# Kernel optimization log

Measured on AMD Instinct MI355X. Metric: run time of the kernel, lower is better.

## Reference

```python
import jax, jax.numpy as jnp
import numpy as np

N = 50000   # nodes
E = 800000  # edges
D = 64      # num_filters == hidden_channels
NG = 5      # num_gaussians (edge_attr width, unused by forward math)
NEG_SLOPE = 0.2


def setup_inputs() -> dict:
    key = jax.random.key(0)
    ks = jax.random.split(key, 16)
    s = 1.0 / np.sqrt(D)
    return {
        "x": jax.random.normal(ks[0], (N, D), dtype=jnp.float32),
        "edge_index": jax.random.randint(ks[1], (2, E), 0, N, dtype=jnp.int64),
        "edge_weight": jax.random.uniform(ks[2], (E,), dtype=jnp.float32),
        "edge_attr": jax.random.normal(ks[3], (E, NG), dtype=jnp.float32),
        "W0": jax.random.normal(ks[4], (D, D), dtype=jnp.float32) * s,
        "b0": jnp.zeros((D,), dtype=jnp.float32),
        "W1": jax.random.normal(ks[5], (D, D), dtype=jnp.float32) * s,
        "as1": jax.random.normal(ks[6], (D,), dtype=jnp.float32) * s,
        "ad1": jax.random.normal(ks[7], (D,), dtype=jnp.float32) * s,
        "b1": jnp.zeros((D,), dtype=jnp.float32),
        "W2": jax.random.normal(ks[8], (D, D), dtype=jnp.float32) * s,
        "as2": jax.random.normal(ks[9], (D,), dtype=jnp.float32) * s,
        "ad2": jax.random.normal(ks[10], (D,), dtype=jnp.float32) * s,
        "b2": jnp.zeros((D,), dtype=jnp.float32),
    }


def gat_layer(h, src, dst, W, a_src, a_dst, b):
    # PyG GATConv, heads=1, add_self_loops=False
    hx = h @ W  # [N, D]
    # per-node attention logits, gathered per edge (edge j->i: src=j, dst=i)
    alpha = (hx * a_src).sum(-1)[src] + (hx * a_dst).sum(-1)[dst]  # [E]
    alpha = jax.nn.leaky_relu(alpha, NEG_SLOPE)
    # segment softmax grouped by destination node
    m = jax.ops.segment_max(alpha, dst, num_segments=N)
    e = jnp.exp(alpha - m[dst])
    s = jax.ops.segment_sum(e, dst, num_segments=N)
    p = e / s[dst]  # [E]
    # scatter-add weighted source features
    out = jax.ops.segment_sum(hx[src] * p[:, None], dst, num_segments=N)
    return out + b


def reference(x, edge_index, edge_weight, edge_attr,
              W0, b0, W1, as1, ad1, b1, W2, as2, ad2, b2):
    # edge_weight / edge_attr are accepted but unused, as in the torch module
    src, dst = edge_index[0], edge_index[1]
    out = jax.nn.relu(x @ W0 + b0)
    out = out + jax.nn.relu(gat_layer(out, src, dst, W1, as1, ad1, b1))
    out = out + jax.nn.relu(gat_layer(out, src, dst, W2, as2, ad2, b2))
    return out
```

## Files before the change

### kernel.cpp

```cpp
#include <hip/hip_runtime.h>
#include <hip/hip_bf16.h>

#define DD 64
#define NEG_SLOPE 0.2f
#define HS 68
#define CAP 64
#define BSH 8
#define BN  256
#define NBMAX 256
#define NBLK 256
#define STAGE_CAP 6144

__device__ __forceinline__ unsigned short f2bf(float f)
{
    unsigned u = __float_as_uint(f);
    u += 0x7FFFu + ((u >> 16) & 1u);
    return (unsigned short)(u >> 16);
}
__device__ __forceinline__ float bf2f(unsigned short b)
{
    return __uint_as_float(((unsigned)b) << 16);
}

__global__ __launch_bounds__(256) void mm_fused(
    const float* __restrict__ x,
    const float* __restrict__ W0, const float* __restrict__ b0,
    const float* __restrict__ W1,
    const float* __restrict__ a_src, const float* __restrict__ a_dst,
    float* __restrict__ h, ushort4* __restrict__ hxb4,
    float* __restrict__ sarr, float* __restrict__ darr, int n)
{
    __shared__ float Wsh[DD * DD];
    __shared__ float Hsh[DD * HS];
    int tid = threadIdx.x;
    for (int i = tid * 4; i < DD * DD; i += 1024)
        *(float4*)&Wsh[i] = *(const float4*)&W0[i];

    int fg = tid & 15, ng = tid >> 4;
    int tile0 = blockIdx.x * 64;
    for (int p = 0; p < 4; ++p) {
        int nl = p * 16 + ng, gn = tile0 + nl;
        if (gn < n)
            *(float4*)&Hsh[nl * HS + 4 * fg] = *(const float4*)&x[gn * DD + 4 * fg];
    }
    __syncthreads();

    float4 acc[4];
#pragma unroll
    for (int j = 0; j < 4; ++j) acc[j] = float4{0.f, 0.f, 0.f, 0.f};
#pragma unroll 8
    for (int k = 0; k < DD; ++k) {
        float4 w4 = *(float4*)&Wsh[k * DD + 4 * fg];
#pragma unroll
        for (int j = 0; j < 4; ++j) {
            float hv = Hsh[(4 * ng + j) * HS + k];
            acc[j].x += hv * w4.x; acc[j].y += hv * w4.y;
            acc[j].z += hv * w4.z; acc[j].w += hv * w4.w;
        }
    }

    float4 b4 = *(const float4*)&b0[4 * fg];
    float4 o[4];
#pragma unroll
    for (int j = 0; j < 4; ++j) {
        o[j].x = fmaxf(acc[j].x + b4.x, 0.f);
        o[j].y = fmaxf(acc[j].y + b4.y, 0.f);
        o[j].z = fmaxf(acc[j].z + b4.z, 0.f);
        o[j].w = fmaxf(acc[j].w + b4.w, 0.f);
        int gn = tile0 + 4 * ng + j;
        if (gn < n) *(float4*)&h[gn * DD + 4 * fg] = o[j];
    }
    __syncthreads();

#pragma unroll
    for (int j = 0; j < 4; ++j)
        *(float4*)&Hsh[(4 * ng + j) * HS + 4 * fg] = o[j];
    for (int i = tid * 4; i < DD * DD; i += 1024)
        *(float4*)&Wsh[i] = *(const float4*)&W1[i];
    __syncthreads();

#pragma unroll
    for (int j = 0; j < 4; ++j) acc[j] = float4{0.f, 0.f, 0.f, 0.f};
#pragma unroll 8
    for (int k = 0; k < DD; ++k) {
        float4 w4 = *(float4*)&Wsh[k * DD + 4 * fg];
#pragma unroll
        for (int j = 0; j < 4; ++j) {
            float hv = Hsh[(4 * ng + j) * HS + k];
            acc[j].x += hv * w4.x; acc[j].y += hv * w4.y;
            acc[j].z += hv * w4.z; acc[j].w += hv * w4.w;
        }
    }

    float4 as4 = *(const float4*)&a_src[4 * fg];
    float4 ad4 = *(const float4*)&a_dst[4 * fg];
#pragma unroll
    for (int j = 0; j < 4; ++j) {
        int gn = tile0 + 4 * ng + j;
        if (gn < n) {
            ushort4 hb;
            hb.x = f2bf(acc[j].x); hb.y = f2bf(acc[j].y);
            hb.z = f2bf(acc[j].z); hb.w = f2bf(acc[j].w);
            hxb4[gn * 16 + fg] = hb;
        }
        float ps = acc[j].x * as4.x + acc[j].y * as4.y + acc[j].z * as4.z + acc[j].w * as4.w;
        float pd = acc[j].x * ad4.x + acc[j].y * ad4.y + acc[j].z * ad4.z + acc[j].w * ad4.w;
#pragma unroll
        for (int off = 8; off; off >>= 1) {
            ps += __shfl_xor(ps, off);
            pd += __shfl_xor(pd, off);
        }
        if (fg == 0 && gn < n) { sarr[gn] = ps; darr[gn] = pd; }
    }
}

__global__ __launch_bounds__(256) void mm_gat(
    const float* __restrict__ h, const float* __restrict__ W,
    const float* __restrict__ a_src, const float* __restrict__ a_dst,
    ushort4* __restrict__ hxb4, float* __restrict__ sarr, float* __restrict__ darr,
    int n)
{
    __shared__ float Wsh[DD * DD];
    __shared__ float Hsh[DD * HS];
    int tid = threadIdx.x;
    for (int i = tid * 4; i < DD * DD; i += 1024)
        *(float4*)&Wsh[i] = *(const float4*)&W[i];

    int fg = tid & 15, ng = tid >> 4;
    int tile0 = blockIdx.x * 64;
    for (int p = 0; p < 4; ++p) {
        int nl = p * 16 + ng, gn = tile0 + nl;
        if (gn < n)
            *(float4*)&Hsh[nl * HS + 4 * fg] = *(const float4*)&h[gn * DD + 4 * fg];
    }
    __syncthreads();

    float4 acc[4];
#pragma unroll
    for (int j = 0; j < 4; ++j) acc[j] = float4{0.f, 0.f, 0.f, 0.f};
#pragma unroll 8
    for (int k = 0; k < DD; ++k) {
        float4 w4 = *(float4*)&Wsh[k * DD + 4 * fg];
#pragma unroll
        for (int j = 0; j < 4; ++j) {
            float hv = Hsh[(4 * ng + j) * HS + k];
            acc[j].x += hv * w4.x; acc[j].y += hv * w4.y;
            acc[j].z += hv * w4.z; acc[j].w += hv * w4.w;
        }
    }

    float4 as4 = *(const float4*)&a_src[4 * fg];
    float4 ad4 = *(const float4*)&a_dst[4 * fg];
#pragma unroll
    for (int j = 0; j < 4; ++j) {
        int gn = tile0 + 4 * ng + j;
        if (gn < n) {
            ushort4 hb;
            hb.x = f2bf(acc[j].x); hb.y = f2bf(acc[j].y);
            hb.z = f2bf(acc[j].z); hb.w = f2bf(acc[j].w);
            hxb4[gn * 16 + fg] = hb;
        }
        float ps = acc[j].x * as4.x + acc[j].y * as4.y + acc[j].z * as4.z + acc[j].w * as4.w;
        float pd = acc[j].x * ad4.x + acc[j].y * ad4.y + acc[j].z * ad4.z + acc[j].w * ad4.w;
#pragma unroll
        for (int off = 8; off; off >>= 1) {
            ps += __shfl_xor(ps, off);
            pd += __shfl_xor(pd, off);
        }
        if (fg == 0 && gn < n) { sarr[gn] = ps; darr[gn] = pd; }
    }
}

__device__ __forceinline__ int wave_incl_scan(int v, int lane)
{
#pragma unroll
    for (int off = 1; off < 64; off <<= 1) {
        int t = __shfl_up(v, off);
        if (lane >= off) v += t;
    }
    return v;
}

__global__ __launch_bounds__(512) void chunk_count(
    const int4* __restrict__ dst4, const int* __restrict__ dst,
    int* __restrict__ cnts, int NB, int E4, int E, int C4)
{
    __shared__ int lh[NBMAX];
    int k = blockIdx.x, tid = threadIdx.x;
    for (int i = tid; i < NB; i += 512) lh[i] = 0;
    __syncthreads();
    int i0 = k * C4, i1 = min(i0 + C4, E4);
    for (int i = i0 + tid; i < i1; i += 512) {
        int4 d = dst4[i];
        atomicAdd(&lh[d.x >> BSH], 1);
        atomicAdd(&lh[d.y >> BSH], 1);
        atomicAdd(&lh[d.z >> BSH], 1);
        atomicAdd(&lh[d.w >> BSH], 1);
    }
    if (k == NBLK - 1) {
        for (int e = E4 * 4 + tid; e < E; e += 512)
            atomicAdd(&lh[dst[e] >> BSH], 1);
    }
    __syncthreads();
    for (int i = tid; i < NB; i += 512) cnts[k * NB + i] = lh[i];
}

__global__ __launch_bounds__(256) void csr_scan(
    const int* __restrict__ cnts, int* __restrict__ boff, int* __restrict__ cbase,
    int* __restrict__ row_ptr, int NB, int N, int E)
{
    __shared__ int wsum[4];
    int t = threadIdx.x, lane = t & 63, w = t >> 6;
    int sum = 0;
    if (t < NB)
        for (int k = 0; k < NBLK; ++k) sum += cnts[k * NB + t];
    int incl = wave_incl_scan(sum, lane);
    if (lane == 63) wsum[w] = incl;
    __syncthreads();
    int wo = 0;
    for (int i = 0; i < w; ++i) wo += wsum[i];
    int excl = wo + incl - sum;
    if (t < NB) {
        boff[t] = excl;
        int run = excl;
        for (int k = 0; k < NBLK; ++k) {
            cbase[k * NB + t] = run;
            run += cnts[k * NB + t];
        }
    }
    if (t == 0) { boff[NB] = E; row_ptr[N] = E; }
}

__global__ __launch_bounds__(512) void chunk_scatter(
    const int4* __restrict__ dst4, const int4* __restrict__ src4,
    const int* __restrict__ dst, const int* __restrict__ src,
    const int* __restrict__ cbase, int* __restrict__ ebuf,
    int NB, int E4, int E, int C4)
{
    __shared__ int lcur[NBMAX];
    int k = blockIdx.x, tid = threadIdx.x;
    for (int i = tid; i < NB; i += 512) lcur[i] = cbase[k * NB + i];
    __syncthreads();
    int i0 = k * C4, i1 = min(i0 + C4, E4);
    for (int i = i0 + tid; i < i1; i += 512) {
        int4 d = dst4[i];
        int4 s = src4[i];
        int b, p;
        b = d.x >> BSH; p = atomicAdd(&lcur[b], 1); ebuf[p] = ((d.x & (BN - 1)) << 24) | s.x;
        b = d.y >> BSH; p = atomicAdd(&lcur[b], 1); ebuf[p] = ((d.y & (BN - 1)) << 24) | s.y;
        b = d.z >> BSH; p = atomicAdd(&lcur[b], 1); ebuf[p] = ((d.z & (BN - 1)) << 24) | s.z;
        b = d.w >> BSH; p = atomicAdd(&lcur[b], 1); ebuf[p] = ((d.w & (BN - 1)) << 24) | s.w;
    }
    if (k == NBLK - 1) {
        for (int e = E4 * 4 + tid; e < E; e += 512) {
            int d = dst[e];
            int b = d >> BSH;
            int p = atomicAdd(&lcur[b], 1);
            ebuf[p] = ((d & (BN - 1)) << 24) | src[e];
        }
    }
}

__global__ __launch_bounds__(512) void group_build(
    const int* __restrict__ ebuf, const int* __restrict__ boff,
    int* __restrict__ row_ptr, int* __restrict__ col, int N)
{
    __shared__ int lcnt[BN];
    __shared__ int loff[BN];
    __shared__ int lcur[BN];
    __shared__ int wsum[4];
    __shared__ int stage[STAGE_CAP];
    int b = blockIdx.x, tid = threadIdx.x;
    int e0 = boff[b], e1 = boff[b + 1];
    int total = e1 - e0;
    if (tid < BN) { lcnt[tid] = 0; lcur[tid] = 0; }
    __syncthreads();
    for (int e = e0 + tid; e < e1; e += 512)
        atomicAdd(&lcnt[((unsigned)ebuf[e]) >> 24], 1);
    __syncthreads();
    int lane = tid & 63, w = tid >> 6;
    int v = (tid < BN) ? lcnt[tid] : 0;
    int incl = wave_incl_scan(v, lane);
    if (tid < BN && lane == 63) wsum[w] = incl;
    __syncthreads();
    if (tid < BN) {
        int wo = 0;
        for (int i = 0; i < w; ++i) wo += wsum[i];
        int excl = wo + incl - v;
        loff[tid] = excl;
        int node = b * BN + tid;
        if (node < N) row_ptr[node] = e0 + excl;
    }
    __syncthreads();
    if (total <= STAGE_CAP) {
        for (int e = e0 + tid; e < e1; e += 512) {
            int p = ebuf[e];
            int dl = ((unsigned)p) >> 24;
            int r = atomicAdd(&lcur[dl], 1);
            stage[loff[dl] + r] = p & 0xFFFFFF;
        }
        __syncthreads();
        for (int i = tid; i < total; i += 512)
            col[e0 + i] = stage[i];
    } else {
        for (int e = e0 + tid; e < e1; e += 512) {
            int p = ebuf[e];
            int dl = ((unsigned)p) >> 24;
            int r = atomicAdd(&lcur[dl], 1);
            col[e0 + loff[dl] + r] = p & 0xFFFFFF;
        }
    }
}

__global__ __launch_bounds__(256) void aggregate(
    const ushort4* __restrict__ hxb4, const int* __restrict__ row_ptr,
    const int* __restrict__ col, const float* __restrict__ sarr,
    const float* __restrict__ darr, const float* __restrict__ bias,
    float* __restrict__ h, int n)
{
    __shared__ float aw[4][CAP];
    __shared__ int   ac[4][CAP];
    int tid = threadIdx.x;
    int wid = tid >> 6, lane = tid & 63, fg = lane & 15, es = lane >> 4;
    int v = blockIdx.x * 4 + wid;
    if (v >= n) return;

    int beg = row_ptr[v], end = row_ptr[v + 1];
    int deg = end - beg;
    float adi = darr[v];
    float m = -3.4e38f, s = 0.f;
    float4 acc = float4{0.f, 0.f, 0.f, 0.f};

    if (deg <= CAP) {
        for (int e = beg + lane; e < end; e += 64) {
            int c = col[e];
            float a = sarr[c] + adi;
            a = a > 0.f ? a : NEG_SLOPE * a;
            ac[wid][e - beg] = c;
            aw[wid][e - beg] = a;
            m = fmaxf(m, a);
        }
#pragma unroll
        for (int off = 32; off; off >>= 1) m = fmaxf(m, __shfl_xor(m, off));
        for (int i = lane; i < deg; i += 64) {
            float w = __expf(aw[wid][i] - m);
            aw[wid][i] = w; s += w;
        }
#pragma unroll
        for (int off = 32; off; off >>= 1) s += __shfl_xor(s, off);
#pragma unroll 2
        for (int i = es; i < deg; i += 4) {
            int c = ac[wid][i];
            float w = aw[wid][i];
            ushort4 u = hxb4[c * 16 + fg];
            acc.x += w * bf2f(u.x); acc.y += w * bf2f(u.y);
            acc.z += w * bf2f(u.z); acc.w += w * bf2f(u.w);
        }
    } else {
        for (int e = beg + lane; e < end; e += 64) {
            float a = sarr[col[e]] + adi;
            a = a > 0.f ? a : NEG_SLOPE * a;
            m = fmaxf(m, a);
        }
#pragma unroll
        for (int off = 32; off; off >>= 1) m = fmaxf(m, __shfl_xor(m, off));
        for (int e = beg + lane; e < end; e += 64) {
            float a = sarr[col[e]] + adi;
            a = a > 0.f ? a : NEG_SLOPE * a;
            s += __expf(a - m);
        }
#pragma unroll
        for (int off = 32; off; off >>= 1) s += __shfl_xor(s, off);
        for (int e = beg + es; e < end; e += 4) {
            int c = col[e];
            float a = sarr[c] + adi;
            a = a > 0.f ? a : NEG_SLOPE * a;
            float w = __expf(a - m);
            ushort4 u = hxb4[c * 16 + fg];
            acc.x += w * bf2f(u.x); acc.y += w * bf2f(u.y);
            acc.z += w * bf2f(u.z); acc.w += w * bf2f(u.w);
        }
    }

    acc.x += __shfl_xor(acc.x, 16); acc.y += __shfl_xor(acc.y, 16);
    acc.z += __shfl_xor(acc.z, 16); acc.w += __shfl_xor(acc.w, 16);
    acc.x += __shfl_xor(acc.x, 32); acc.y += __shfl_xor(acc.y, 32);
    acc.z += __shfl_xor(acc.z, 32); acc.w += __shfl_xor(acc.w, 32);

    if (es == 0) {
        float inv = (s > 0.f) ? 1.f / s : 0.f;
        float4 b4 = ((const float4*)bias)[fg];
        float4 o;
        o.x = fmaxf(acc.x * inv + b4.x, 0.f);
        o.y = fmaxf(acc.y * inv + b4.y, 0.f);
        o.z = fmaxf(acc.z * inv + b4.z, 0.f);
        o.w = fmaxf(acc.w * inv + b4.w, 0.f);
        float4* hp = (float4*)&h[v * DD + 4 * fg];
        float4 cur = *hp;
        cur.x += o.x; cur.y += o.y; cur.z += o.z; cur.w += o.w;
        *hp = cur;
    }
}

extern "C" void kernel_launch(void* const* d_in, const int* in_sizes, int n_in,
                              void* d_out, int out_size, void* d_ws, size_t ws_size,
                              hipStream_t stream)
{
    const float* x  = (const float*)d_in[0];
    const int*   ei = (const int*)d_in[1];
    const float* W0 = (const float*)d_in[4];
    const float* b0 = (const float*)d_in[5];
    const float* W1 = (const float*)d_in[6];
    const float* as1= (const float*)d_in[7];
    const float* ad1= (const float*)d_in[8];
    const float* b1 = (const float*)d_in[9];
    const float* W2 = (const float*)d_in[10];
    const float* as2= (const float*)d_in[11];
    const float* ad2= (const float*)d_in[12];
    const float* b2 = (const float*)d_in[13];

    int N = in_sizes[0] / DD;
    int E = in_sizes[1] / 2;
    int E4 = E >> 2;
    int C4 = (E4 + NBLK - 1) / NBLK;
    int NB = (N + BN - 1) >> BSH;
    float* h = (float*)d_out;

    ushort4* hxb4 = (ushort4*)d_ws;
    float* sarr   = (float*)(hxb4 + (size_t)N * 16);
    float* darr   = sarr + N;
    int*   row_ptr= (int*)(darr + N);
    int*   cnts   = row_ptr + (N + 1);
    int*   cbase  = cnts + NBLK * NB;
    int*   boff   = cbase + NBLK * NB;
    int*   ebuf   = boff + (NB + 1);
    int*   colb   = ebuf + E;

    const int* src = ei;
    const int* dst = ei + E;
    const int4* dst4 = (const int4*)dst;
    const int4* src4 = (const int4*)src;

    int mm_tiles = (N + 63) / 64;
    int agg_blks = (N + 3) / 4;

    chunk_count<<<NBLK, 512, 0, stream>>>(dst4, dst, cnts, NB, E4, E, C4);
    csr_scan<<<1, 256, 0, stream>>>(cnts, boff, cbase, row_ptr, NB, N, E);
    chunk_scatter<<<NBLK, 512, 0, stream>>>(dst4, src4, dst, src, cbase, ebuf, NB, E4, E, C4);
    group_build<<<NB, 512, 0, stream>>>(ebuf, boff, row_ptr, colb, N);

    mm_fused<<<mm_tiles, 256, 0, stream>>>(x, W0, b0, W1, as1, ad1, h, hxb4, sarr, darr, N);
    aggregate<<<agg_blks, 256, 0, stream>>>(hxb4, row_ptr, colb, sarr, darr, b1, h, N);

    mm_gat<<<mm_tiles, 256, 0, stream>>>(h, W2, as2, ad2, hxb4, sarr, darr, N);
    aggregate<<<agg_blks, 256, 0, stream>>>(hxb4, row_ptr, colb, sarr, darr, b2, h, N);
}
```

Before: 216.5 us.

## Fuse edge counting with first matmul and layer-1 aggregation with second matmul

Merges the chunk_count histogram and the first fused matmul into one launch, with block index selecting the role. It also fuses the first GAT aggregation with the second layer's projection so the updated node features go straight into shared memory for the matmul, using double-buffered hx/s/d arrays. The CSR scan is parallelized across 16 waves with shuffle reductions and scans. These changes cut kernel launches and a full re-read of h, at the cost of larger blocks, more shared memory, and lower occupancy in the fused aggregation kernel.

```diff
diff --git a/kernel.cpp b/kernel.cpp
--- a/kernel.cpp
+++ b/kernel.cpp
@@ -1,5 +1,4 @@
 #include <hip/hip_runtime.h>
-#include <hip/hip_bf16.h>
 
 #define DD 64
 #define NEG_SLOPE 0.2f
@@ -10,6 +9,7 @@
 #define NBMAX 256
 #define NBLK 256
 #define STAGE_CAP 6144
+#define AMM_NODES 32
 
 __device__ __forceinline__ unsigned short f2bf(float f)
 {
@@ -22,71 +22,106 @@
     return __uint_as_float(((unsigned)b) << 16);
 }
 
-__global__ __launch_bounds__(256) void mm_fused(
-    const float* __restrict__ x,
-    const float* __restrict__ W0, const float* __restrict__ b0,
-    const float* __restrict__ W1,
+__device__ __forceinline__ int wave_incl_scan(int v, int lane)
+{
+#pragma unroll
+    for (int off = 1; off < 64; off <<= 1) {
+        int t = __shfl_up(v, off);
+        if (lane >= off) v += t;
+    }
+    return v;
+}
+
+__global__ __launch_bounds__(512) void count_mm(
+    const int4* __restrict__ dst4, const int* __restrict__ dst,
+    int* __restrict__ cnts, int NB, int E4, int E, int C4,
+    const float* __restrict__ x, const float* __restrict__ W0,
+    const float* __restrict__ b0, const float* __restrict__ W1,
     const float* __restrict__ a_src, const float* __restrict__ a_dst,
     float* __restrict__ h, ushort4* __restrict__ hxb4,
     float* __restrict__ sarr, float* __restrict__ darr, int n)
 {
-    __shared__ float Wsh[DD * DD];
-    __shared__ float Hsh[DD * HS];
+    __shared__ float smem[DD * DD + DD * HS];
     int tid = threadIdx.x;
-    for (int i = tid * 4; i < DD * DD; i += 1024)
+
+    if (blockIdx.x < NBLK) {
+        int* lh = (int*)smem;
+        int k = blockIdx.x;
+        for (int i = tid; i < NB; i += 512) lh[i] = 0;
+        __syncthreads();
+        int i0 = k * C4, i1 = min(i0 + C4, E4);
+        for (int i = i0 + tid; i < i1; i += 512) {
+            int4 d = dst4[i];
+            atomicAdd(&lh[d.x >> BSH], 1);
+            atomicAdd(&lh[d.y >> BSH], 1);
+            atomicAdd(&lh[d.z >> BSH], 1);
+            atomicAdd(&lh[d.w >> BSH], 1);
+        }
+        if (k == NBLK - 1) {
+            for (int e = E4 * 4 + tid; e < E; e += 512)
+                atomicAdd(&lh[dst[e] >> BSH], 1);
+        }
+        __syncthreads();
+        for (int i = tid; i < NB; i += 512) cnts[k * NB + i] = lh[i];
+        return;
+    }
+
+    float* Wsh = smem;
+    float* Hsh = smem + DD * DD;
+    int fg = tid & 15, ng = tid >> 4;
+    int tile0 = (blockIdx.x - NBLK) * 64;
+
+    for (int i = tid * 4; i < DD * DD; i += 2048)
         *(float4*)&Wsh[i] = *(const float4*)&W0[i];
-
-    int fg = tid & 15, ng = tid >> 4;
-    int tile0 = blockIdx.x * 64;
-    for (int p = 0; p < 4; ++p) {
-        int nl = p * 16 + ng, gn = tile0 + nl;
+    for (int p = 0; p < 2; ++p) {
+        int nl = p * 32 + ng, gn = tile0 + nl;
         if (gn < n)
             *(float4*)&Hsh[nl * HS + 4 * fg] = *(const float4*)&x[gn * DD + 4 * fg];
     }
     __syncthreads();
 
-    float4 acc[4];
-#pragma unroll
-    for (int j = 0; j < 4; ++j) acc[j] = float4{0.f, 0.f, 0.f, 0.f};
+    float4 acc[2];
+#pragma unroll
+    for (int j = 0; j < 2; ++j) acc[j] = float4{0.f, 0.f, 0.f, 0.f};
 #pragma unroll 8
     for (int k = 0; k < DD; ++k) {
         float4 w4 = *(float4*)&Wsh[k * DD + 4 * fg];
 #pragma unroll
-        for (int j = 0; j < 4; ++j) {
-            float hv = Hsh[(4 * ng + j) * HS + k];
+        for (int j = 0; j < 2; ++j) {
+            float hv = Hsh[(2 * ng + j) * HS + k];
             acc[j].x += hv * w4.x; acc[j].y += hv * w4.y;
             acc[j].z += hv * w4.z; acc[j].w += hv * w4.w;
         }
     }
 
     float4 b4 = *(const float4*)&b0[4 * fg];
-    float4 o[4];
-#pragma unroll
-    for (int j = 0; j < 4; ++j) {
+    float4 o[2];
+#pragma unroll
+    for (int j = 0; j < 2; ++j) {
         o[j].x = fmaxf(acc[j].x + b4.x, 0.f);
         o[j].y = fmaxf(acc[j].y + b4.y, 0.f);
         o[j].z = fmaxf(acc[j].z + b4.z, 0.f);
         o[j].w = fmaxf(acc[j].w + b4.w, 0.f);
-        int gn = tile0 + 4 * ng + j;
+        int gn = tile0 + 2 * ng + j;
         if (gn < n) *(float4*)&h[gn * DD + 4 * fg] = o[j];
     }
     __syncthreads();
 
 #pragma unroll
-    for (int j = 0; j < 4; ++j)
-        *(float4*)&Hsh[(4 * ng + j) * HS + 4 * fg] = o[j];
-    for (int i = tid * 4; i < DD * DD; i += 1024)
+    for (int j = 0; j < 2; ++j)
+        *(float4*)&Hsh[(2 * ng + j) * HS + 4 * fg] = o[j];
+    for (int i = tid * 4; i < DD * DD; i += 2048)
         *(float4*)&Wsh[i] = *(const float4*)&W1[i];
     __syncthreads();
 
 #pragma unroll
-    for (int j = 0; j < 4; ++j) acc[j] = float4{0.f, 0.f, 0.f, 0.f};
+    for (int j = 0; j < 2; ++j) acc[j] = float4{0.f, 0.f, 0.f, 0.f};
 #pragma unroll 8
     for (int k = 0; k < DD; ++k) {
         float4 w4 = *(float4*)&Wsh[k * DD + 4 * fg];
 #pragma unroll
-        for (int j = 0; j < 4; ++j) {
-            float hv = Hsh[(4 * ng + j) * HS + k];
+        for (int j = 0; j < 2; ++j) {
+            float hv = Hsh[(2 * ng + j) * HS + k];
             acc[j].x += hv * w4.x; acc[j].y += hv * w4.y;
             acc[j].z += hv * w4.z; acc[j].w += hv * w4.w;
         }
@@ -95,8 +130,8 @@
     float4 as4 = *(const float4*)&a_src[4 * fg];
     float4 ad4 = *(const float4*)&a_dst[4 * fg];
 #pragma unroll
-    for (int j = 0; j < 4; ++j) {
-        int gn = tile0 + 4 * ng + j;
+    for (int j = 0; j < 2; ++j) {
+        int gn = tile0 + 2 * ng + j;
         if (gn < n) {
             ushort4 hb;
             hb.x = f2bf(acc[j].x); hb.y = f2bf(acc[j].y);
@@ -114,121 +149,49 @@
     }
 }
 
-__global__ __launch_bounds__(256) void mm_gat(
-    const float* __restrict__ h, const float* __restrict__ W,
-    const float* __restrict__ a_src, const float* __restrict__ a_dst,
-    ushort4* __restrict__ hxb4, float* __restrict__ sarr, float* __restrict__ darr,
-    int n)
-{
-    __shared__ float Wsh[DD * DD];
-    __shared__ float Hsh[DD * HS];
-    int tid = threadIdx.x;
-    for (int i = tid * 4; i < DD * DD; i += 1024)
-        *(float4*)&Wsh[i] = *(const float4*)&W[i];
-
-    int fg = tid & 15, ng = tid >> 4;
-    int tile0 = blockIdx.x * 64;
-    for (int p = 0; p < 4; ++p) {
-        int nl = p * 16 + ng, gn = tile0 + nl;
-        if (gn < n)
-            *(float4*)&Hsh[nl * HS + 4 * fg] = *(const float4*)&h[gn * DD + 4 * fg];
-    }
-    __syncthreads();
-
-    float4 acc[4];
-#pragma unroll
-    for (int j = 0; j < 4; ++j) acc[j] = float4{0.f, 0.f, 0.f, 0.f};
-#pragma unroll 8
-    for (int k = 0; k < DD; ++k) {
-        float4 w4 = *(float4*)&Wsh[k * DD + 4 * fg];
-#pragma unroll
-        for (int j = 0; j < 4; ++j) {
-            float hv = Hsh[(4 * ng + j) * HS + k];
-            acc[j].x += hv * w4.x; acc[j].y += hv * w4.y;
-            acc[j].z += hv * w4.z; acc[j].w += hv * w4.w;
-        }
-    }
-
-    float4 as4 = *(const float4*)&a_src[4 * fg];
-    float4 ad4 = *(const float4*)&a_dst[4 * fg];
-#pragma unroll
-    for (int j = 0; j < 4; ++j) {
-        int gn = tile0 + 4 * ng + j;
-        if (gn < n) {
-            ushort4 hb;
-            hb.x = f2bf(acc[j].x); hb.y = f2bf(acc[j].y);
-            hb.z = f2bf(acc[j].z); hb.w = f2bf(acc[j].w);
-            hxb4[gn * 16 + fg] = hb;
-        }
-        float ps = acc[j].x * as4.x + acc[j].y * as4.y + acc[j].z * as4.z + acc[j].w * as4.w;
-        float pd = acc[j].x * ad4.x + acc[j].y * ad4.y + acc[j].z * ad4.z + acc[j].w * ad4.w;
-#pragma unroll
-        for (int off = 8; off; off >>= 1) {
-            ps += __shfl_xor(ps, off);
-            pd += __shfl_xor(pd, off);
-        }
-        if (fg == 0 && gn < n) { sarr[gn] = ps; darr[gn] = pd; }
-    }
-}
-
-__device__ __forceinline__ int wave_incl_scan(int v, int lane)
-{
-#pragma unroll
-    for (int off = 1; off < 64; off <<= 1) {
-        int t = __shfl_up(v, off);
-        if (lane >= off) v += t;
-    }
-    return v;
-}
-
-__global__ __launch_bounds__(512) void chunk_count(
-    const int4* __restrict__ dst4, const int* __restrict__ dst,
-    int* __restrict__ cnts, int NB, int E4, int E, int C4)
-{
-    __shared__ int lh[NBMAX];
-    int k = blockIdx.x, tid = threadIdx.x;
-    for (int i = tid; i < NB; i += 512) lh[i] = 0;
-    __syncthreads();
-    int i0 = k * C4, i1 = min(i0 + C4, E4);
-    for (int i = i0 + tid; i < i1; i += 512) {
-        int4 d = dst4[i];
-        atomicAdd(&lh[d.x >> BSH], 1);
-        atomicAdd(&lh[d.y >> BSH], 1);
-        atomicAdd(&lh[d.z >> BSH], 1);
-        atomicAdd(&lh[d.w >> BSH], 1);
-    }
-    if (k == NBLK - 1) {
-        for (int e = E4 * 4 + tid; e < E; e += 512)
-            atomicAdd(&lh[dst[e] >> BSH], 1);
-    }
-    __syncthreads();
-    for (int i = tid; i < NB; i += 512) cnts[k * NB + i] = lh[i];
-}
-
-__global__ __launch_bounds__(256) void csr_scan(
+__global__ __launch_bounds__(1024) void csr_scan(
     const int* __restrict__ cnts, int* __restrict__ boff, int* __restrict__ cbase,
     int* __restrict__ row_ptr, int NB, int N, int E)
 {
+    __shared__ int tot[NBMAX];
+    __shared__ int sbo[NBMAX];
     __shared__ int wsum[4];
-    int t = threadIdx.x, lane = t & 63, w = t >> 6;
-    int sum = 0;
-    if (t < NB)
-        for (int k = 0; k < NBLK; ++k) sum += cnts[k * NB + t];
-    int incl = wave_incl_scan(sum, lane);
-    if (lane == 63) wsum[w] = incl;
-    __syncthreads();
-    int wo = 0;
-    for (int i = 0; i < w; ++i) wo += wsum[i];
-    int excl = wo + incl - sum;
-    if (t < NB) {
-        boff[t] = excl;
-        int run = excl;
-        for (int k = 0; k < NBLK; ++k) {
-            cbase[k * NB + t] = run;
-            run += cnts[k * NB + t];
-        }
-    }
-    if (t == 0) { boff[NB] = E; row_ptr[N] = E; }
+    int tid = threadIdx.x, lane = tid & 63, w = tid >> 6;
+
+    for (int b = w; b < NB; b += 16) {
+        int s0 = 0;
+#pragma unroll
+        for (int s = 0; s < NBLK; s += 64) s0 += cnts[(s + lane) * NB + b];
+#pragma unroll
+        for (int off = 32; off; off >>= 1) s0 += __shfl_xor(s0, off);
+        if (lane == 0) tot[b] = s0;
+    }
+    __syncthreads();
+
+    int v = 0;
+    if (tid < 256) v = (tid < NB) ? tot[tid] : 0;
+    int incl = wave_incl_scan(v, lane);
+    if (tid < 256 && lane == 63) wsum[w] = incl;
+    __syncthreads();
+    if (tid < 256) {
+        int wo = 0;
+        for (int i = 0; i < w; ++i) wo += wsum[i];
+        int excl = wo + incl - v;
+        if (tid < NB) { sbo[tid] = excl; boff[tid] = excl; }
+    }
+    if (tid == 0) { boff[NB] = E; row_ptr[N] = E; }
+    __syncthreads();
+
+    for (int b = w; b < NB; b += 16) {
+        int carry = sbo[b];
+#pragma unroll
+        for (int s = 0; s < NBLK; s += 64) {
+            int c = cnts[(s + lane) * NB + b];
+            int incl2 = wave_incl_scan(c, lane);
+            cbase[(s + lane) * NB + b] = carry + incl2 - c;
+            carry += __shfl(incl2, 63);
+        }
+    }
 }
 
 __global__ __launch_bounds__(512) void chunk_scatter(
@@ -310,6 +273,138 @@
             col[e0 + loff[dl] + r] = p & 0xFFFFFF;
         }
     }
+}
+
+__global__ __launch_bounds__(512) void agg_mm(
+    const ushort4* __restrict__ hxA, const int* __restrict__ row_ptr,
+    const int* __restrict__ col, const float* __restrict__ sA,
+    const float* __restrict__ dA, const float* __restrict__ bias,
+    float* __restrict__ h, const float* __restrict__ W,
+    const float* __restrict__ a_src, const float* __restrict__ a_dst,
+    ushort4* __restrict__ hxB, float* __restrict__ sB, float* __restrict__ dB,
+    int n)
+{
+    __shared__ float Wsh[DD * DD];
+    __shared__ float Hsh[AMM_NODES * HS];
+    __shared__ float aw[8][CAP];
+    __shared__ int   ac[8][CAP];
+    int tid = threadIdx.x;
+    int w = tid >> 6, lane = tid & 63, fg = lane & 15, es = lane >> 4;
+    int tile0 = blockIdx.x * AMM_NODES;
+
+    for (int i = tid * 4; i < DD * DD; i += 2048)
+        *(float4*)&Wsh[i] = *(const float4*)&W[i];
+
+    for (int q = 0; q < 4; ++q) {
+        int nl = 4 * w + q;
+        int v = tile0 + nl;
+        if (v >= n) continue;
+
+        int beg = row_ptr[v], end = row_ptr[v + 1];
+        int deg = end - beg;
+        float adi = dA[v];
+        float m = -3.4e38f, s = 0.f;
+        float4 acc = float4{0.f, 0.f, 0.f, 0.f};
+
+        if (deg <= CAP) {
+            for (int e = beg + lane; e < end; e += 64) {
+                int c = col[e];
+                float a = sA[c] + adi;
+                a = a > 0.f ? a : NEG_SLOPE * a;
+                ac[w][e - beg] = c;
+                aw[w][e - beg] = a;
+                m = fmaxf(m, a);
+            }
+#pragma unroll
+            for (int off = 32; off; off >>= 1) m = fmaxf(m, __shfl_xor(m, off));
+            for (int i = lane; i < deg; i += 64) {
+                float wv = __expf(aw[w][i] - m);
+                aw[w][i] = wv; s += wv;
+            }
+#pragma unroll
+            for (int off = 32; off; off >>= 1) s += __shfl_xor(s, off);
+#pragma unroll 2
+            for (int i = es; i < deg; i += 4) {
+                int c = ac[w][i];
+                float wv = aw[w][i];
+                ushort4 u = hxA[c * 16 + fg];
+                acc.x += wv * bf2f(u.x); acc.y += wv * bf2f(u.y);
+                acc.z += wv * bf2f(u.z); acc.w += wv * bf2f(u.w);
+            }
+        } else {
+            for (int e = beg + lane; e < end; e += 64) {
+                float a = sA[col[e]] + adi;
+                a = a > 0.f ? a : NEG_SLOPE * a;
+                m = fmaxf(m, a);
+            }
+#pragma unroll
+            for (int off = 32; off; off >>= 1) m = fmaxf(m, __shfl_xor(m, off));
+            for (int e = beg + lane; e < end; e += 64) {
+                float a = sA[col[e]] + adi;
+                a = a > 0.f ? a : NEG_SLOPE * a;
+                s += __expf(a - m);
+            }
+#pragma unroll
+            for (int off = 32; off; off >>= 1) s += __shfl_xor(s, off);
+            for (int e = beg + es; e < end; e += 4) {
+                int c = col[e];
+                float a = sA[c] + adi;
+                a = a > 0.f ? a : NEG_SLOPE * a;
+                float wv = __expf(a - m);
+                ushort4 u = hxA[c * 16 + fg];
+                acc.x += wv * bf2f(u.x); acc.y += wv * bf2f(u.y);
+                acc.z += wv * bf2f(u.z); acc.w += wv * bf2f(u.w);
+            }
+        }
+
+        acc.x += __shfl_xor(acc.x, 16); acc.y += __shfl_xor(acc.y, 16);
+        acc.z += __shfl_xor(acc.z, 16); acc.w += __shfl_xor(acc.w, 16);
+        acc.x += __shfl_xor(acc.x, 32); acc.y += __shfl_xor(acc.y, 32);
+        acc.z += __shfl_xor(acc.z, 32); acc.w += __shfl_xor(acc.w, 32);
+
+        if (es == 0) {
+            float inv = (s > 0.f) ? 1.f / s : 0.f;
+            float4 b4 = ((const float4*)bias)[fg];
+            float4 o;
+            o.x = fmaxf(acc.x * inv + b4.x, 0.f);
+            o.y = fmaxf(acc.y * inv + b4.y, 0.f);
+            o.z = fmaxf(acc.z * inv + b4.z, 0.f);
+            o.w = fmaxf(acc.w * inv + b4.w, 0.f);
+            float4* hp = (float4*)&h[v * DD + 4 * fg];
+            float4 cur = *hp;
+            cur.x += o.x; cur.y += o.y; cur.z += o.z; cur.w += o.w;
+            *hp = cur;
+            *(float4*)&Hsh[nl * HS + 4 * fg] = cur;
+        }
+    }
+    __syncthreads();
+
+    int nl2 = tid >> 4;
+    float4 acc2 = float4{0.f, 0.f, 0.f, 0.f};
+#pragma unroll 8
+    for (int k = 0; k < DD; ++k) {
+        float4 w4 = *(float4*)&Wsh[k * DD + 4 * fg];
+        float hv = Hsh[nl2 * HS + k];
+        acc2.x += hv * w4.x; acc2.y += hv * w4.y;
+        acc2.z += hv * w4.z; acc2.w += hv * w4.w;
+    }
+    int gn = tile0 + nl2;
+    float4 as4 = *(const float4*)&a_src[4 * fg];
+    float4 ad4 = *(const float4*)&a_dst[4 * fg];
+    if (gn < n) {
+        ushort4 hb;
+        hb.x = f2bf(acc2.x); hb.y = f2bf(acc2.y);
+        hb.z = f2bf(acc2.z); hb.w = f2bf(acc2.w);
+        hxB[gn * 16 + fg] = hb;
+    }
+    float ps = acc2.x * as4.x + acc2.y * as4.y + acc2.z * as4.z + acc2.w * as4.w;
+    float pd = acc2.x * ad4.x + acc2.y * ad4.y + acc2.z * ad4.z + acc2.w * ad4.w;
+#pragma unroll
+    for (int off = 8; off; off >>= 1) {
+        ps += __shfl_xor(ps, off);
+        pd += __shfl_xor(pd, off);
+    }
+    if (fg == 0 && gn < n) { sB[gn] = ps; dB[gn] = pd; }
 }
 
 __global__ __launch_bounds__(256) void aggregate(
@@ -426,10 +521,13 @@
     int NB = (N + BN - 1) >> BSH;
     float* h = (float*)d_out;
 
-    ushort4* hxb4 = (ushort4*)d_ws;
-    float* sarr   = (float*)(hxb4 + (size_t)N * 16);
-    float* darr   = sarr + N;
-    int*   row_ptr= (int*)(darr + N);
+    ushort4* hxA  = (ushort4*)d_ws;
+    ushort4* hxB  = hxA + (size_t)N * 16;
+    float* sA     = (float*)(hxB + (size_t)N * 16);
+    float* dA     = sA + N;
+    float* sB     = dA + N;
+    float* dB     = sB + N;
+    int*   row_ptr= (int*)(dB + N);
     int*   cnts   = row_ptr + (N + 1);
     int*   cbase  = cnts + NBLK * NB;
     int*   boff   = cbase + NBLK * NB;
@@ -441,17 +539,17 @@
     const int4* dst4 = (const int4*)dst;
     const int4* src4 = (const int4*)src;
 
-    int mm_tiles = (N + 63) / 64;
-    int agg_blks = (N + 3) / 4;
-
-    chunk_count<<<NBLK, 512, 0, stream>>>(dst4, dst, cnts, NB, E4, E, C4);
-    csr_scan<<<1, 256, 0, stream>>>(cnts, boff, cbase, row_ptr, NB, N, E);
+    int mm_tiles  = (N + 63) / 64;
+    int amm_blks  = (N + AMM_NODES - 1) / AMM_NODES;
+    int agg_blks  = (N + 3) / 4;
+
+    count_mm<<<NBLK + mm_tiles, 512, 0, stream>>>(
+        dst4, dst, cnts, NB, E4, E, C4,
+        x, W0, b0, W1, as1, ad1, h, hxA, sA, dA, N);
+    csr_scan<<<1, 1024, 0, stream>>>(cnts, boff, cbase, row_ptr, NB, N, E);
     chunk_scatter<<<NBLK, 512, 0, stream>>>(dst4, src4, dst, src, cbase, ebuf, NB, E4, E, C4);
     group_build<<<NB, 512, 0, stream>>>(ebuf, boff, row_ptr, colb, N);
-
-    mm_fused<<<mm_tiles, 256, 0, stream>>>(x, W0, b0, W1, as1, ad1, h, hxb4, sarr, darr, N);
-    aggregate<<<agg_blks, 256, 0, stream>>>(hxb4, row_ptr, colb, sarr, darr, b1, h, N);
-
-    mm_gat<<<mm_tiles, 256, 0, stream>>>(h, W2, as2, ad2, hxb4, sarr, darr, N);
-    aggregate<<<agg_blks, 256, 0, stream>>>(hxb4, row_ptr, colb, sarr, darr, b2, h, N);
-}
+    agg_mm<<<amm_blks, 512, 0, stream>>>(hxA, row_ptr, colb, sA, dA, b1,
+                                         h, W2, as2, ad2, hxB, sB, dB, N);
+    aggregate<<<agg_blks, 256, 0, stream>>>(hxB, row_ptr, colb, sB, dB, b2, h, N);
+}
```

Result: slower. 280.3 us (+29.5%).
